# Kernel optimization log

Measured on AMD Instinct MI355X. Metric: run time of the kernel, lower is better.

The kernel has to match this reference:

```python
import jax, jax.numpy as jnp
import numpy as np

IN_FEATURES = 4096
OUT_FEATURES = 11008
BLOCK_SIZE = 64

NF4_TABLE = jnp.array([-1.0, -0.6961928009986877, -0.5250730514526367, -0.39491748809814453,
                       -0.28444138169288635, -0.18477343022823334, -0.09105003625154495, 0.0,
                       0.07958029955625534, 0.16093020141124725, 0.24611230194568634,
                       0.33791524171829224, 0.44070982933044434, 0.5626170039176941,
                       0.7229568362236023, 1.0], dtype=jnp.float32)


def setup_inputs() -> dict:
    key = jax.random.key(0)
    k1, k2, k3, k4 = jax.random.split(key, 4)
    n = IN_FEATURES * OUT_FEATURES
    x = jax.random.normal(k1, (4, 128, IN_FEATURES), dtype=jnp.float32)
    # packed 4-bit codes: two codes per byte, flat layout as produced by quantize_and_pack_nf4
    packed_kernel = jax.random.randint(k2, (n // 2,), 0, 256, dtype=jnp.int32).astype(jnp.uint8)
    # per-block absmax scales (positive)
    scales = jax.random.uniform(k3, (n // BLOCK_SIZE,), minval=0.01, maxval=0.05, dtype=jnp.float32)
    bias = jax.random.normal(k4, (OUT_FEATURES,), dtype=jnp.float32) * 0.01
    return {"x": x, "packed_kernel": packed_kernel, "scales": scales, "bias": bias}


def _dequantize_nf4(packed, absmax, block_size):
    high = (packed >> 4) & 15
    low = packed & 15
    # interleave: [h0, l0, h1, l1, ...] matching jnp.stack([high, low], axis=1).reshape(-1)
    unpacked = jnp.stack([high, low], axis=1).reshape(-1)
    deq = NF4_TABLE[unpacked]                       # [n] fp32
    deq = deq.reshape(-1, block_size) * absmax[:, None]  # per-block scaling
    return deq


def reference(x, packed_kernel, scales, bias):
    kernel = _dequantize_nf4(packed_kernel, scales, BLOCK_SIZE).reshape(IN_FEATURES, OUT_FEATURES)
    y = jnp.einsum("bsi,io->bso", x, kernel)
    y = y + bias
    return y
```

## Files before the change

### kernel.cpp

```cpp
#include <hip/hip_runtime.h>
#include <hip/hip_bf16.h>
#include <hip/hip_fp16.h>
#include <stdint.h>

#define K_DIM 4096
#define N_DIM 11008
#define M_DIM 512
#define PK_ROW 5504
#define SC_ROW 172

typedef __attribute__((ext_vector_type(4))) float f32x4;
typedef __attribute__((ext_vector_type(4))) int i32x4;
typedef __attribute__((ext_vector_type(4))) unsigned int u32x4;
typedef __attribute__((ext_vector_type(8))) _Float16 half8;
typedef __attribute__((ext_vector_type(8))) short bf16x8;

__constant__ float NF4[16] = {
    -1.0f, -0.6961928009986877f, -0.5250730514526367f, -0.39491748809814453f,
    -0.28444138169288635f, -0.18477343022823334f, -0.09105003625154495f, 0.0f,
    0.07958029955625534f, 0.16093020141124725f, 0.24611230194568634f,
    0.33791524171829224f, 0.44070982933044434f, 0.5626170039176941f,
    0.7229568362236023f, 1.0f};

union H8 { u32x4 v; half8 h; };

__device__ __forceinline__ unsigned h2mul(unsigned a, unsigned b) {
  union { __half2 h; unsigned u; } x, y, r;
  x.u = a; y.u = b;
  r.h = x.h * y.h;
  return r.u;
}
__device__ __forceinline__ unsigned hpack(float a, float b) {
  union { __half2 h; unsigned u; } c;
  c.h = __floats2half2_rn(a, b);
  return c.u;
}
__device__ __forceinline__ unsigned f2bf(float v) {
  union { __hip_bfloat16 h; unsigned short u; } cv;
  cv.h = __float2bfloat16(v);
  return (unsigned)cv.u;
}

__global__ __launch_bounds__(256) void conv_a16(const float* __restrict__ x,
                                                unsigned* __restrict__ wsa) {
  const int wid = blockIdx.x * 4 + (threadIdx.x >> 6);
  const int lane = threadIdx.x & 63;
  const int m16 = wid >> 7, k32 = wid & 127;
  const int m = m16 * 16 + (lane & 15);
  const int k = k32 * 32 + (lane >> 4) * 8;
  const float* src = x + (size_t)m * K_DIM + k;
  f32x4 v0 = *(const f32x4*)src;
  f32x4 v1 = *(const f32x4*)(src + 4);
  u32x4 d;
  d[0] = hpack(v0[0], v0[1]);
  d[1] = hpack(v0[2], v0[3]);
  d[2] = hpack(v1[0], v1[1]);
  d[3] = hpack(v1[2], v1[3]);
  *(u32x4*)(wsa + (size_t)wid * 256 + lane * 4) = d;
}

__global__ __launch_bounds__(256) void prep_codes(const int* __restrict__ packed,
                                                  unsigned* __restrict__ codes) {
  const int b = blockIdx.x;
  const int kt = b & 63;
  const int nt = b >> 6;
  __shared__ unsigned char Sb[128 * 36];
  const int t = threadIdx.x;
  const int npl = t & 63;
  const int kq = t >> 6;
  const int np = nt * 64 + npl;
#pragma unroll
  for (int i = 0; i < 8; ++i) {
    const int kpl = kq + i * 4;
    const int k = kt * 64 + kpl * 2;
    const int w0 = packed[(size_t)k * PK_ROW + np];
    const int w1 = packed[(size_t)(k + 1) * PK_ROW + np];
    Sb[(npl * 2) * 36 + kpl] =
        (unsigned char)((((w0 >> 4) & 15) << 4) | ((w1 >> 4) & 15));
    Sb[(npl * 2 + 1) * 36 + kpl] =
        (unsigned char)(((w0 & 15) << 4) | (w1 & 15));
  }
  __syncthreads();
#pragma unroll
  for (int i = 0; i < 4; ++i) {
    const int lin = t + 256 * i;
    const int n16 = lin & 15;
    const int kp4l = (lin >> 4) & 7;
    const int nb16l = lin >> 7;
    const unsigned v = *(const unsigned*)(Sb + (nb16l * 16 + n16) * 36 + kp4l * 4);
    const size_t D = ((size_t)(nt * 8 + nb16l) * 512 + kt * 8 + kp4l) * 16 + n16;
    codes[D] = v;
  }
}

__global__ __launch_bounds__(256) void prep_scales(const float* __restrict__ scales,
                                                   unsigned* __restrict__ scalesp) {
  const int g = blockIdx.x * 256 + threadIdx.x;
  if (g >= SC_ROW * 2048) return;
  const int kp = g / SC_ROW;
  const int nb = g - kp * SC_ROW;
  const float s0 = scales[(size_t)(2 * kp) * SC_ROW + nb];
  const float s1 = scales[(size_t)(2 * kp + 1) * SC_ROW + nb];
  scalesp[(size_t)nb * 2048 + kp] = hpack(s0, s1);
}

template <int KS>
__global__ __launch_bounds__(256, 3) void nf4_gemm16(
    const unsigned* __restrict__ codes, const unsigned* __restrict__ scalesp,
    const unsigned* __restrict__ wsa, const float* __restrict__ bias,
    float* __restrict__ cout) {
  __shared__ unsigned LutR[256 * 32];

  const int bid = blockIdx.x;
  const int x = bid & 7;
  const int local = bid >> 3;
  const int kh = (KS == 2) ? (local & 1) : 0;
  const int q = (KS == 2) ? (local >> 1) : local;
  const int tile = x * 43 + q;
  const int m_tile = (tile / 86) * 128;
  const int n_tile = (tile % 86) * 128;

  const int t = threadIdx.x;
  {
    const int c = t & 31;
    const int b0 = t >> 5;
#pragma unroll
    for (int i = 0; i < 32; ++i) {
      const int b = b0 + 8 * i;
      LutR[b * 32 + c] = hpack(NF4[(b >> 4) & 15], NF4[b & 15]);
    }
  }
  __syncthreads();

  const int lane = t & 63;
  const int wid = t >> 6;
  const int wm2 = wid >> 1;
  const int wnh = wid & 1;
  const int l15 = lane & 15;
  const int kslice = lane >> 4;
  const int lb = lane & 31;
  const int m16w = (m_tile >> 4) + wm2 * 4;
  const int nf0 = (n_tile >> 4) + wnh * 4;
  const int nb64 = (n_tile >> 6) + wnh;

  unsigned cb[4];
#pragma unroll
  for (int j = 0; j < 4; ++j) cb[j] = (unsigned)(nf0 + j) * 8192 + lane;
  const unsigned sb = (unsigned)nb64 * 2048 + kslice * 4;
  unsigned ab[4];
#pragma unroll
  for (int fm = 0; fm < 4; ++fm)
    ab[fm] = (unsigned)(m16w + fm) * 32768 + lane * 4;

  f32x4 acc[4][4];
#pragma unroll
  for (int i = 0; i < 4; ++i)
#pragma unroll
    for (int j = 0; j < 4; ++j) acc[i][j] = (f32x4){0.f, 0.f, 0.f, 0.f};

  const int NS = 128 / KS;
  const int s_base = kh * NS;

  auto LOAD = [&](int sl, unsigned* c, u32x4& sv, u32x4* A) {
    const unsigned s = (unsigned)(s_base + sl);
#pragma unroll
    for (int j = 0; j < 4; ++j) c[j] = codes[cb[j] + 64u * s];
    sv = *(const u32x4*)(scalesp + sb + 16u * s);
#pragma unroll
    for (int fm = 0; fm < 4; ++fm)
      A[fm] = *(const u32x4*)(wsa + ab[fm] + 256u * s);
  };
  auto STEP = [&](const unsigned* c, const u32x4& sv, const u32x4* A) {
    H8 a[4];
#pragma unroll
    for (int fm = 0; fm < 4; ++fm) a[fm].v = A[fm];
#pragma unroll
    for (int j = 0; j < 4; ++j) {
      const unsigned cw = c[j];
      H8 B;
      B.v[0] = h2mul(LutR[((cw & 255u) << 5) | lb], sv[0]);
      B.v[1] = h2mul(LutR[(((cw >> 8) & 255u) << 5) | lb], sv[1]);
      B.v[2] = h2mul(LutR[(((cw >> 16) & 255u) << 5) | lb], sv[2]);
      B.v[3] = h2mul(LutR[((cw >> 24) << 5) | lb], sv[3]);
#pragma unroll
      for (int fm = 0; fm < 4; ++fm)
        acc[fm][j] = __builtin_amdgcn_mfma_f32_16x16x32_f16(a[fm].h, B.h, acc[fm][j], 0, 0, 0);
    }
  };

  unsigned Xc[4], Yc[4];
  u32x4 Xs, Ys;
  u32x4 XA[4], YA[4];
  LOAD(0, Xc, Xs, XA);
#pragma unroll 1
  for (int s = 0; s < NS; s += 2) {
    LOAD(s + 1, Yc, Ys, YA);
    STEP(Xc, Xs, XA);
    if (s + 2 < NS) LOAD(s + 2, Xc, Xs, XA);
    STEP(Yc, Ys, YA);
  }

  float* dst = cout + (KS == 2 ? (size_t)kh * ((size_t)M_DIM * N_DIM) : 0);
#pragma unroll
  for (int j = 0; j < 4; ++j) {
    const int gc = n_tile + wnh * 64 + j * 16 + l15;
    const float bi = (KS == 1) ? bias[gc] : 0.f;
#pragma unroll
    for (int fm = 0; fm < 4; ++fm) {
#pragma unroll
      for (int r = 0; r < 4; ++r) {
        const int gr = m_tile + wm2 * 64 + fm * 16 + kslice * 4 + r;
        dst[(size_t)gr * N_DIM + gc] = acc[fm][j][r] + bi;
      }
    }
  }
}

__global__ __launch_bounds__(256) void reduce_bias(
    const float* __restrict__ c0, const float* __restrict__ c1,
    const float* __restrict__ bias, float* __restrict__ out) {
  const int tot4 = (M_DIM * N_DIM) / 4;
  const int stride = gridDim.x * 256;
  for (int i = blockIdx.x * 256 + threadIdx.x; i < tot4; i += stride) {
    const int e0 = i * 4;
    const int col = e0 % N_DIM;
    f32x4 a = *(const f32x4*)(c0 + e0);
    f32x4 b = *(const f32x4*)(c1 + e0);
    f32x4 bi = *(const f32x4*)(bias + col);
    *(f32x4*)(out + e0) = a + b + bi;
  }
}

#define FLDS 72
__global__ __launch_bounds__(256) void nf4_gemm_fused(
    const float* __restrict__ x, const int* __restrict__ packed,
    const float* __restrict__ scales, const float* __restrict__ bias,
    float* __restrict__ out) {
  __shared__ unsigned short AldsF[128 * FLDS];
  __shared__ unsigned short BldsF[128 * FLDS];
  __shared__ float2 Lut[256];
  const int t = threadIdx.x;
  const int bid = blockIdx.x;
  const int swz = (bid & 7) * 43 + (bid >> 3);
  const int m_tile = (swz / 86) * 128;
  const int n_tile = (swz % 86) * 128;
  Lut[t] = make_float2(NF4[(t >> 4) & 15], NF4[t & 15]);
  const int lane = t & 63;
  const int wid = t >> 6;
  const int wm = (wid >> 1) * 64;
  const int wn = (wid & 1) * 64;
  const int l15 = lane & 15;
  const int l4 = lane >> 4;
  f32x4 acc[4][4];
#pragma unroll
  for (int i = 0; i < 4; ++i)
#pragma unroll
    for (int j = 0; j < 4; ++j) acc[i][j] = (f32x4){0.f, 0.f, 0.f, 0.f};
  const int mlane = t & 15;
  const int n_sub = mlane * 8;
  const int k_sub = 4 * (((t >> 4) + mlane) & 15);
  const int c4 = t & 15;
  const int r0 = t >> 4;
  for (int k0 = 0; k0 < K_DIM; k0 += 64) {
    __syncthreads();
#pragma unroll
    for (int i = 0; i < 8; ++i) {
      const int row = r0 + 16 * i;
      f32x4 xv = *(const f32x4*)(x + (size_t)(m_tile + row) * K_DIM + k0 + c4 * 4);
      uint2 d;
      d.x = f2bf(xv[0]) | (f2bf(xv[1]) << 16);
      d.y = f2bf(xv[2]) | (f2bf(xv[3]) << 16);
      *(uint2*)(&AldsF[row * FLDS + c4 * 4]) = d;
    }
    {
      const int* pk = packed + (size_t)(k0 + k_sub) * PK_ROW + ((n_tile + n_sub) >> 1);
      i32x4 w[4];
      float s[4];
#pragma unroll
      for (int kk = 0; kk < 4; ++kk) {
        w[kk] = *(const i32x4*)(pk + (size_t)kk * PK_ROW);
        s[kk] = scales[(size_t)(k0 + k_sub + kk) * SC_ROW + ((n_tile + n_sub) >> 6)];
      }
      float v[4][8];
#pragma unroll
      for (int kk = 0; kk < 4; ++kk)
#pragma unroll
        for (int e = 0; e < 4; ++e) {
          const int b = w[kk][e] & 0xFF;
          const float2 p = Lut[b];
          v[kk][2 * e] = p.x * s[kk];
          v[kk][2 * e + 1] = p.y * s[kk];
        }
#pragma unroll
      for (int j = 0; j < 8; ++j) {
        uint2 d;
        d.x = f2bf(v[0][j]) | (f2bf(v[1][j]) << 16);
        d.y = f2bf(v[2][j]) | (f2bf(v[3][j]) << 16);
        *(uint2*)(&BldsF[(n_sub + j) * FLDS + k_sub]) = d;
      }
    }
    __syncthreads();
#pragma unroll
    for (int ks = 0; ks < 2; ++ks) {
      bf16x8 af[4], bfv[4];
#pragma unroll
      for (int fm = 0; fm < 4; ++fm)
        af[fm] = *(const bf16x8*)(&AldsF[(wm + fm * 16 + l15) * FLDS + ks * 32 + l4 * 8]);
#pragma unroll
      for (int fn = 0; fn < 4; ++fn)
        bfv[fn] = *(const bf16x8*)(&BldsF[(wn + fn * 16 + l15) * FLDS + ks * 32 + l4 * 8]);
#pragma unroll
      for (int fm = 0; fm < 4; ++fm)
#pragma unroll
        for (int fn = 0; fn < 4; ++fn)
          acc[fm][fn] = __builtin_amdgcn_mfma_f32_16x16x32_bf16(af[fm], bfv[fn], acc[fm][fn], 0, 0, 0);
    }
  }
#pragma unroll
  for (int fn = 0; fn < 4; ++fn) {
    const float bi = bias[n_tile + wn + fn * 16 + l15];
#pragma unroll
    for (int fm = 0; fm < 4; ++fm)
#pragma unroll
      for (int r = 0; r < 4; ++r) {
        const int gr = m_tile + wm + fm * 16 + l4 * 4 + r;
        out[(size_t)gr * N_DIM + n_tile + wn + fn * 16 + l15] = acc[fm][fn][r] + bi;
      }
  }
}

extern "C" void kernel_launch(void* const* d_in, const int* in_sizes, int n_in,
                              void* d_out, int out_size, void* d_ws, size_t ws_size,
                              hipStream_t stream) {
  const float* x = (const float*)d_in[0];
  const int* packed = (const int*)d_in[1];
  const float* scales = (const float*)d_in[2];
  const float* bias = (const float*)d_in[3];
  float* out = (float*)d_out;

  const size_t A_BYTES = (size_t)M_DIM * K_DIM * 2;
  const size_t C_BYTES = (size_t)688 * 512 * 16 * 4;
  const size_t S_BYTES = (size_t)SC_ROW * 2048 * 4;
  const size_t P_BYTES = (size_t)2 * M_DIM * N_DIM * 4;
  const size_t need1 = A_BYTES + C_BYTES + S_BYTES;
  const size_t need2 = need1 + P_BYTES;

  if (ws_size >= need1) {
    unsigned* wsa = (unsigned*)d_ws;
    unsigned* codes = (unsigned*)((char*)d_ws + A_BYTES);
    unsigned* scalesp = (unsigned*)((char*)d_ws + A_BYTES + C_BYTES);
    conv_a16<<<dim3(1024), dim3(256), 0, stream>>>(x, wsa);
    prep_codes<<<dim3(5504), dim3(256), 0, stream>>>(packed, codes);
    prep_scales<<<dim3(1376), dim3(256), 0, stream>>>(scales, scalesp);
    if (ws_size >= need2) {
      float* cpart = (float*)((char*)d_ws + need1);
      nf4_gemm16<2><<<dim3(688), dim3(256), 0, stream>>>(codes, scalesp, wsa, bias, cpart);
      reduce_bias<<<dim3(2048), dim3(256), 0, stream>>>(
          cpart, cpart + (size_t)M_DIM * N_DIM, bias, out);
    } else {
      nf4_gemm16<1><<<dim3(344), dim3(256), 0, stream>>>(codes, scalesp, wsa, bias, out);
    }
  } else {
    nf4_gemm_fused<<<dim3(344), dim3(256), 0, stream>>>(x, packed, scales, bias, out);
  }
}
```

Before: 102.2 us.

## Merge prep kernels, use 4-way split-K with atomic accumulation, add setprio

Folds the three preprocessing kernels into one launch that picks its branch by block index. The GEMM now splits K four ways instead of two and accumulates partial sums straight into the zeroed output with float atomics. This removes the separate reduce kernel and the partial-sum workspace. It adds a memset, four atomic writes per output element, a nondeterministic summation order, and s_setprio around the MFMA section.

```diff
diff --git a/kernel.cpp b/kernel.cpp
--- a/kernel.cpp
+++ b/kernel.cpp
@@ -41,81 +41,79 @@
   return (unsigned)cv.u;
 }
 
-__global__ __launch_bounds__(256) void conv_a16(const float* __restrict__ x,
-                                                unsigned* __restrict__ wsa) {
-  const int wid = blockIdx.x * 4 + (threadIdx.x >> 6);
-  const int lane = threadIdx.x & 63;
-  const int m16 = wid >> 7, k32 = wid & 127;
-  const int m = m16 * 16 + (lane & 15);
-  const int k = k32 * 32 + (lane >> 4) * 8;
-  const float* src = x + (size_t)m * K_DIM + k;
-  f32x4 v0 = *(const f32x4*)src;
-  f32x4 v1 = *(const f32x4*)(src + 4);
-  u32x4 d;
-  d[0] = hpack(v0[0], v0[1]);
-  d[1] = hpack(v0[2], v0[3]);
-  d[2] = hpack(v1[0], v1[1]);
-  d[3] = hpack(v1[2], v1[3]);
-  *(u32x4*)(wsa + (size_t)wid * 256 + lane * 4) = d;
-}
-
-__global__ __launch_bounds__(256) void prep_codes(const int* __restrict__ packed,
-                                                  unsigned* __restrict__ codes) {
-  const int b = blockIdx.x;
-  const int kt = b & 63;
-  const int nt = b >> 6;
-  __shared__ unsigned char Sb[128 * 36];
+__global__ __launch_bounds__(256) void prep_all(
+    const float* __restrict__ x, const int* __restrict__ packed,
+    const float* __restrict__ scales, unsigned* __restrict__ wsa,
+    unsigned* __restrict__ codes, unsigned* __restrict__ scalesp) {
+  const int bid = blockIdx.x;
   const int t = threadIdx.x;
-  const int npl = t & 63;
-  const int kq = t >> 6;
-  const int np = nt * 64 + npl;
-#pragma unroll
-  for (int i = 0; i < 8; ++i) {
-    const int kpl = kq + i * 4;
-    const int k = kt * 64 + kpl * 2;
-    const int w0 = packed[(size_t)k * PK_ROW + np];
-    const int w1 = packed[(size_t)(k + 1) * PK_ROW + np];
-    Sb[(npl * 2) * 36 + kpl] =
-        (unsigned char)((((w0 >> 4) & 15) << 4) | ((w1 >> 4) & 15));
-    Sb[(npl * 2 + 1) * 36 + kpl] =
-        (unsigned char)(((w0 & 15) << 4) | (w1 & 15));
-  }
-  __syncthreads();
-#pragma unroll
-  for (int i = 0; i < 4; ++i) {
-    const int lin = t + 256 * i;
-    const int n16 = lin & 15;
-    const int kp4l = (lin >> 4) & 7;
-    const int nb16l = lin >> 7;
-    const unsigned v = *(const unsigned*)(Sb + (nb16l * 16 + n16) * 36 + kp4l * 4);
-    const size_t D = ((size_t)(nt * 8 + nb16l) * 512 + kt * 8 + kp4l) * 16 + n16;
-    codes[D] = v;
-  }
-}
-
-__global__ __launch_bounds__(256) void prep_scales(const float* __restrict__ scales,
-                                                   unsigned* __restrict__ scalesp) {
-  const int g = blockIdx.x * 256 + threadIdx.x;
-  if (g >= SC_ROW * 2048) return;
-  const int kp = g / SC_ROW;
-  const int nb = g - kp * SC_ROW;
-  const float s0 = scales[(size_t)(2 * kp) * SC_ROW + nb];
-  const float s1 = scales[(size_t)(2 * kp + 1) * SC_ROW + nb];
-  scalesp[(size_t)nb * 2048 + kp] = hpack(s0, s1);
-}
-
-template <int KS>
+  if (bid < 5504) {
+    const int kt = bid & 63;
+    const int nt = bid >> 6;
+    __shared__ unsigned char Sb[128 * 36];
+    const int npl = t & 63;
+    const int kq = t >> 6;
+    const int np = nt * 64 + npl;
+#pragma unroll
+    for (int i = 0; i < 8; ++i) {
+      const int kpl = kq + i * 4;
+      const int k = kt * 64 + kpl * 2;
+      const int w0 = packed[(size_t)k * PK_ROW + np];
+      const int w1 = packed[(size_t)(k + 1) * PK_ROW + np];
+      Sb[(npl * 2) * 36 + kpl] =
+          (unsigned char)((((w0 >> 4) & 15) << 4) | ((w1 >> 4) & 15));
+      Sb[(npl * 2 + 1) * 36 + kpl] =
+          (unsigned char)(((w0 & 15) << 4) | (w1 & 15));
+    }
+    __syncthreads();
+#pragma unroll
+    for (int i = 0; i < 4; ++i) {
+      const int lin = t + 256 * i;
+      const int n16 = lin & 15;
+      const int kp4l = (lin >> 4) & 7;
+      const int nb16l = lin >> 7;
+      const unsigned v = *(const unsigned*)(Sb + (nb16l * 16 + n16) * 36 + kp4l * 4);
+      const size_t D = ((size_t)(nt * 8 + nb16l) * 512 + kt * 8 + kp4l) * 16 + n16;
+      codes[D] = v;
+    }
+  } else if (bid < 6528) {
+    const int wid = (bid - 5504) * 4 + (t >> 6);
+    const int lane = t & 63;
+    const int m16 = wid >> 7, k32 = wid & 127;
+    const int m = m16 * 16 + (lane & 15);
+    const int k = k32 * 32 + (lane >> 4) * 8;
+    const float* src = x + (size_t)m * K_DIM + k;
+    f32x4 v0 = *(const f32x4*)src;
+    f32x4 v1 = *(const f32x4*)(src + 4);
+    u32x4 d;
+    d[0] = hpack(v0[0], v0[1]);
+    d[1] = hpack(v0[2], v0[3]);
+    d[2] = hpack(v1[0], v1[1]);
+    d[3] = hpack(v1[2], v1[3]);
+    *(u32x4*)(wsa + (size_t)wid * 256 + lane * 4) = d;
+  } else {
+    const int g = (bid - 6528) * 256 + t;
+    if (g < SC_ROW * 2048) {
+      const int kp = g / SC_ROW;
+      const int nb = g - kp * SC_ROW;
+      const float s0 = scales[(size_t)(2 * kp) * SC_ROW + nb];
+      const float s1 = scales[(size_t)(2 * kp + 1) * SC_ROW + nb];
+      scalesp[(size_t)nb * 2048 + kp] = hpack(s0, s1);
+    }
+  }
+}
+
 __global__ __launch_bounds__(256, 3) void nf4_gemm16(
     const unsigned* __restrict__ codes, const unsigned* __restrict__ scalesp,
     const unsigned* __restrict__ wsa, const float* __restrict__ bias,
-    float* __restrict__ cout) {
+    float* __restrict__ out) {
   __shared__ unsigned LutR[256 * 32];
 
   const int bid = blockIdx.x;
   const int x = bid & 7;
   const int local = bid >> 3;
-  const int kh = (KS == 2) ? (local & 1) : 0;
-  const int q = (KS == 2) ? (local >> 1) : local;
+  const int kh = local & 3;
+  const int q = local >> 2;
   const int tile = x * 43 + q;
   const int m_tile = (tile / 86) * 128;
   const int n_tile = (tile % 86) * 128;
@@ -158,7 +156,7 @@
 #pragma unroll
     for (int j = 0; j < 4; ++j) acc[i][j] = (f32x4){0.f, 0.f, 0.f, 0.f};
 
-  const int NS = 128 / KS;
+  const int NS = 32;
   const int s_base = kh * NS;
 
   auto LOAD = [&](int sl, unsigned* c, u32x4& sv, u32x4* A) {
@@ -174,6 +172,7 @@
     H8 a[4];
 #pragma unroll
     for (int fm = 0; fm < 4; ++fm) a[fm].v = A[fm];
+    __builtin_amdgcn_s_setprio(1);
 #pragma unroll
     for (int j = 0; j < 4; ++j) {
       const unsigned cw = c[j];
@@ -186,6 +185,7 @@
       for (int fm = 0; fm < 4; ++fm)
         acc[fm][j] = __builtin_amdgcn_mfma_f32_16x16x32_f16(a[fm].h, B.h, acc[fm][j], 0, 0, 0);
     }
+    __builtin_amdgcn_s_setprio(0);
   };
 
   unsigned Xc[4], Yc[4];
@@ -200,34 +200,18 @@
     STEP(Yc, Ys, YA);
   }
 
-  float* dst = cout + (KS == 2 ? (size_t)kh * ((size_t)M_DIM * N_DIM) : 0);
 #pragma unroll
   for (int j = 0; j < 4; ++j) {
     const int gc = n_tile + wnh * 64 + j * 16 + l15;
-    const float bi = (KS == 1) ? bias[gc] : 0.f;
+    const float bi = (kh == 0) ? bias[gc] : 0.f;
 #pragma unroll
     for (int fm = 0; fm < 4; ++fm) {
 #pragma unroll
       for (int r = 0; r < 4; ++r) {
         const int gr = m_tile + wm2 * 64 + fm * 16 + kslice * 4 + r;
-        dst[(size_t)gr * N_DIM + gc] = acc[fm][j][r] + bi;
+        unsafeAtomicAdd(&out[(size_t)gr * N_DIM + gc], acc[fm][j][r] + bi);
       }
     }
-  }
-}
-
-__global__ __launch_bounds__(256) void reduce_bias(
-    const float* __restrict__ c0, const float* __restrict__ c1,
-    const float* __restrict__ bias, float* __restrict__ out) {
-  const int tot4 = (M_DIM * N_DIM) / 4;
-  const int stride = gridDim.x * 256;
-  for (int i = blockIdx.x * 256 + threadIdx.x; i < tot4; i += stride) {
-    const int e0 = i * 4;
-    const int col = e0 % N_DIM;
-    f32x4 a = *(const f32x4*)(c0 + e0);
-    f32x4 b = *(const f32x4*)(c1 + e0);
-    f32x4 bi = *(const f32x4*)(bias + col);
-    *(f32x4*)(out + e0) = a + b + bi;
   }
 }
 
@@ -341,25 +325,15 @@
   const size_t A_BYTES = (size_t)M_DIM * K_DIM * 2;
   const size_t C_BYTES = (size_t)688 * 512 * 16 * 4;
   const size_t S_BYTES = (size_t)SC_ROW * 2048 * 4;
-  const size_t P_BYTES = (size_t)2 * M_DIM * N_DIM * 4;
-  const size_t need1 = A_BYTES + C_BYTES + S_BYTES;
-  const size_t need2 = need1 + P_BYTES;
-
-  if (ws_size >= need1) {
+  const size_t need = A_BYTES + C_BYTES + S_BYTES;
+
+  if (ws_size >= need) {
     unsigned* wsa = (unsigned*)d_ws;
     unsigned* codes = (unsigned*)((char*)d_ws + A_BYTES);
     unsigned* scalesp = (unsigned*)((char*)d_ws + A_BYTES + C_BYTES);
-    conv_a16<<<dim3(1024), dim3(256), 0, stream>>>(x, wsa);
-    prep_codes<<<dim3(5504), dim3(256), 0, stream>>>(packed, codes);
-    prep_scales<<<dim3(1376), dim3(256), 0, stream>>>(scales, scalesp);
-    if (ws_size >= need2) {
-      float* cpart = (float*)((char*)d_ws + need1);
-      nf4_gemm16<2><<<dim3(688), dim3(256), 0, stream>>>(codes, scalesp, wsa, bias, cpart);
-      reduce_bias<<<dim3(2048), dim3(256), 0, stream>>>(
-          cpart, cpart + (size_t)M_DIM * N_DIM, bias, out);
-    } else {
-      nf4_gemm16<1><<<dim3(344), dim3(256), 0, stream>>>(codes, scalesp, wsa, bias, out);
-    }
+    hipMemsetAsync(out, 0, (size_t)out_size * 4, stream);
+    prep_all<<<dim3(7904), dim3(256), 0, stream>>>(x, packed, scales, wsa, codes, scalesp);
+    nf4_gemm16<<<dim3(1376), dim3(256), 0, stream>>>(codes, scalesp, wsa, bias, out);
   } else {
     nf4_gemm_fused<<<dim3(344), dim3(256), 0, stream>>>(x, packed, scales, bias, out);
   }
```

Result: slower. 144.9 us (+41.8%).
